# Kernel optimization log

Hardware: AMD Instinct MI355X
Metric: run time of the kernel (lower is better)

## Reference

```python
import jax, jax.numpy as jnp
import numpy as np
import math

B, N, E = 256, 512, 2048          # graphs, nodes per graph, edges per graph
EMB = 64                           # emb_sz (must be 64 to match final per-graph matmul with 64-d fc2 output)
NUM_ITEMS, NUM_CATS = 400000, 1000
RATIO = 0.9
EPS = 1e-5


def _bn(x, g, b):
    # BatchNorm1d in training mode: biased batch statistics
    m = x.mean(axis=0)
    v = x.var(axis=0)
    return g * (x - m) * jax.lax.rsqrt(v + EPS) + b


def _graph_conv(x, src, dst, emask, Wr, Wn, b):
    # PyG GraphConv, aggr='add': out_i = lin_root(x_i) + lin_rel(sum_{j->i} x_j) + bias
    msg = jnp.where(emask[:, None], x[src], jnp.zeros((), x.dtype))  # [E_tot, C]
    agg = jnp.zeros_like(x).at[dst].add(msg)
    return agg @ Wn + x @ Wr + b


def _topk_pool(x, src, dst, emask, p, n):
    # TopKPooling: score = x.p/||p||, keep top ceil(ratio*n) per graph, gate with tanh(score)
    k = int(math.ceil(RATIO * n))
    score = x @ p / jnp.linalg.norm(p)                       # [B*n]
    _, idx = jax.lax.top_k(score.reshape(B, n), k)           # [B, k] local indices
    gidx = (idx + (jnp.arange(B) * n)[:, None]).reshape(-1)  # [B*k] global indices
    xk = x[gidx] * jnp.tanh(score[gidx])[:, None]
    # remap edges; edges touching a dropped node become masked-out
    mapping = jnp.full((B * n,), -1, jnp.int32).at[gidx].set(jnp.arange(B * k, dtype=jnp.int32))
    nsrc, ndst = mapping[src], mapping[dst]
    valid = (nsrc >= 0) & (ndst >= 0) & emask
    return xk, jnp.maximum(nsrc, 0), jnp.maximum(ndst, 0), valid, k


def _readout(x, k):
    # uniform graphs: global_max_pool / global_mean_pool via reshape
    xg = x.reshape(B, k, -1)
    return jnp.concatenate([xg.max(axis=1), xg.mean(axis=1)], axis=1)  # [B, 256]


def setup_inputs() -> dict:
    key = jax.random.key(0)
    ks = jax.random.split(key, 32)
    nrm = jax.random.normal
    s = 0.02
    item_id = jax.random.randint(ks[0], (B * N,), 0, NUM_ITEMS)
    cat_id = jax.random.randint(ks[1], (B * N,), 0, NUM_CATS)
    off = (jnp.arange(B, dtype=jnp.int32) * N)[:, None]
    src = (jax.random.randint(ks[2], (B, E), 0, N, dtype=jnp.int32) + off).reshape(-1)
    dst = (jax.random.randint(ks[3], (B, E), 0, N, dtype=jnp.int32) + off).reshape(-1)
    d = dict(
        item_id=item_id, cat_id=cat_id, src=src, dst=dst,
        emb_item=nrm(ks[4], (NUM_ITEMS, EMB)) * s,
        emb_cat=nrm(ks[5], (NUM_CATS, EMB)) * s,
        W1r=nrm(ks[6], (2 * EMB, 128)) * s, W1n=nrm(ks[7], (2 * EMB, 128)) * s, b1=jnp.zeros(128), p1=nrm(ks[8], (128,)),
        W2r=nrm(ks[9], (128, 128)) * s, W2n=nrm(ks[10], (128, 128)) * s, b2=jnp.zeros(128), p2=nrm(ks[11], (128,)),
        W3r=nrm(ks[12], (128, 128)) * s, W3n=nrm(ks[13], (128, 128)) * s, b3=jnp.zeros(128), p3=nrm(ks[14], (128,)),
        fc1_W=nrm(ks[15], (256, 128)) * s, fc1_b=jnp.zeros(128), bn1_g=jnp.ones(128), bn1_b=jnp.zeros(128),
        fc2_W=nrm(ks[16], (128, 64)) * s, fc2_b=jnp.zeros(64), bn2_g=jnp.ones(64), bn2_b=jnp.zeros(64),
    )
    return d


def reference(item_id, cat_id, src, dst, emb_item, emb_cat,
              W1r, W1n, b1, p1, W2r, W2n, b2, p2, W3r, W3n, b3, p3,
              fc1_W, fc1_b, bn1_g, bn1_b, fc2_W, fc2_b, bn2_g, bn2_b):
    e_item = emb_item[item_id]                               # [B*N, 64]
    e_cat = emb_cat[cat_id]                                  # [B*N, 64]
    x = jnp.concatenate([e_item, e_cat], axis=1)             # [B*N, 128]
    emask = jnp.ones(src.shape, bool)

    x = jax.nn.relu(_graph_conv(x, src, dst, emask, W1r, W1n, b1))
    x, src, dst, emask, k1 = _topk_pool(x, src, dst, emask, p1, N)
    x1 = _readout(x, k1)

    x = jax.nn.relu(_graph_conv(x, src, dst, emask, W2r, W2n, b2))
    x, src, dst, emask, k2 = _topk_pool(x, src, dst, emask, p2, k1)
    x2 = _readout(x, k2)

    x = jax.nn.relu(_graph_conv(x, src, dst, emask, W3r, W3n, b3))
    x, src, dst, emask, k3 = _topk_pool(x, src, dst, emask, p3, k2)
    x3 = _readout(x, k3)

    g = x1 + x2 + x3                                         # [B, 256]
    g = jax.nn.relu(_bn(g @ fc1_W + fc1_b, bn1_g, bn1_b))    # fc1
    g = jax.nn.relu(_bn(g @ fc2_W + fc2_b, bn2_g, bn2_b))    # fc2
    # dropout is identity in eval; original applies relu again after dropout
    g = jax.nn.relu(g)                                       # [B, 64]
    # per-graph matmul loop: out[n] = <emb_item[n], g[graph_of_n]>; uniform graphs -> einsum
    out = jnp.einsum('bnd,bd->bn', e_item.reshape(B, N, EMB), g).reshape(-1)
    return jax.nn.sigmoid(out)                               # [B*N]
```

## Files before the change

### kernel.cpp

```cpp
#include <hip/hip_runtime.h>
#include <hip/hip_bf16.h>
#include <math.h>


#define TOTAL_NODES 131072
#define NUM_GRAPHS  256
#define NODES_PER_G 512
#define E_TOTAL     524288
#define EPG         2048
#define FDIM        128
#define EMBD        64

typedef __bf16 bf16x8 __attribute__((ext_vector_type(8)));
typedef float  f32x4  __attribute__((ext_vector_type(4)));

static __device__ __forceinline__ f32x4 mfma16(bf16x8 a, bf16x8 b, f32x4 c) {
  return __builtin_amdgcn_mfma_f32_16x16x32_bf16(a, b, c, 0, 0, 0);
}

static inline size_t align256(size_t x) { return (x + 255) & ~size_t(255); }

__global__ __launch_bounds__(256) void gather_embed_k(
    const int* __restrict__ item_id, const int* __restrict__ cat_id,
    const float* __restrict__ emb_item, const float* __restrict__ emb_cat,
    float* __restrict__ x, int total)
{
  int i = blockIdx.x * 256 + threadIdx.x;
  int node = i >> 5, part = i & 31;
  if (node >= total) return;
  float4 v;
  if (part < 16) {
    v = *(const float4*)&emb_item[(size_t)item_id[node] * EMBD + part * 4];
  } else {
    v = *(const float4*)&emb_cat[(size_t)cat_id[node] * EMBD + (part - 16) * 4];
  }
  *(float4*)&x[(size_t)node * FDIM + part * 4] = v;
}

__global__ __launch_bounds__(256) void wprep_k(
    const float* __restrict__ w0, const float* __restrict__ w1,
    const float* __restrict__ w2, const float* __restrict__ w3,
    const float* __restrict__ w4, const float* __restrict__ w5,
    __bf16* __restrict__ wout)
{
  const float* ws[6] = {w0, w1, w2, w3, w4, w5};
  int mat = blockIdx.y;
  int idx = blockIdx.x * 256 + threadIdx.x;
  int n = idx >> 7, k = idx & 127;
  float v = ws[mat][k * FDIM + n];
  __bf16 h = (__bf16)v;
  __bf16 l = (__bf16)(v - (float)h);
  __bf16* base = wout + (size_t)mat * 2 * 16384;
  base[idx] = h;
  base[16384 + idx] = l;
}

__global__ __launch_bounds__(128) void pnorm3_k(
    const float* __restrict__ p1, const float* __restrict__ p2,
    const float* __restrict__ p3, float* __restrict__ nrm)
{
  __shared__ float ss[128];
  const float* ps[3] = {p1, p2, p3};
  int t = threadIdx.x;
  for (int m = 0; m < 3; ++m) {
    float v = ps[m][t];
    ss[t] = v * v;
    __syncthreads();
    for (int s = 64; s > 0; s >>= 1) {
      if (t < s) ss[t] += ss[t + s];
      __syncthreads();
    }
    if (t == 0) nrm[m] = sqrtf(ss[0]);
    __syncthreads();
  }
}

__global__ __launch_bounds__(512) void csr_build1_k(
    const int* __restrict__ src_in, const int* __restrict__ dst_in,
    int* __restrict__ src_out, int* __restrict__ dst_out,
    int2* __restrict__ slot_pack, int* __restrict__ counts, int* __restrict__ offs)
{
  __shared__ int hist[512];
  __shared__ int scn[512];
  __shared__ int cur[512];
  const int b = blockIdx.x, t = threadIdx.x;
  const int ebase = b * EPG;
  const int nbase = b * NODES_PER_G;
  hist[t] = 0;
  __syncthreads();
  int so[4], ld[4];
#pragma unroll
  for (int i = 0; i < 4; ++i) {
    int e = ebase + t + i * 512;
    int s = src_in[e] - nbase;
    int d = dst_in[e] - nbase;
    src_out[e] = s; dst_out[e] = d;
    so[i] = s; ld[i] = d;
    atomicAdd(&hist[d], 1);
  }
  __syncthreads();
  int v = hist[t];
  scn[t] = v;
  __syncthreads();
  for (int dd = 1; dd < 512; dd <<= 1) {
    int add = (t >= dd) ? scn[t - dd] : 0;
    __syncthreads();
    scn[t] += add;
    __syncthreads();
  }
  {
    int excl = scn[t] - v;
    counts[nbase + t] = v;
    offs[nbase + t] = ebase + excl;
    cur[t] = excl;
  }
  __syncthreads();
#pragma unroll
  for (int i = 0; i < 4; ++i) {
    int pos = atomicAdd(&cur[ld[i]], 1);
    slot_pack[ebase + pos] = make_int2(nbase + so[i], __float_as_int(1.0f));
  }
}

__global__ __launch_bounds__(256) void gather_direct_k(
    const float* __restrict__ x, const int2* __restrict__ slot_pack,
    const int* __restrict__ off, const int* __restrict__ counts,
    float* __restrict__ agg, int M)
{
  int i = blockIdx.x * 256 + threadIdx.x;
  int node = i >> 5, lane = i & 31;
  if (node >= M) return;
  int deg = counts[node];
  int base = off[node];
  float4 a = make_float4(0.f, 0.f, 0.f, 0.f);
  for (int d = 0; d < deg; ++d) {
    int2 sp = slot_pack[base + d];
    float gt = __int_as_float(sp.y);
    float4 v = *(const float4*)&x[(size_t)sp.x * FDIM + lane * 4];
    a.x += gt * v.x; a.y += gt * v.y; a.z += gt * v.z; a.w += gt * v.w;
  }
  *(float4*)&agg[(size_t)node * FDIM + lane * 4] = a;
}

__global__ __launch_bounds__(256) void conv_mfma_k(
    const float* __restrict__ Asrc, const int* __restrict__ sel,
    const float* __restrict__ gates,
    const __bf16* __restrict__ W1hl,
    const float* __restrict__ A2,
    const __bf16* __restrict__ W2hl,
    const float* __restrict__ bias, const float* __restrict__ p,
    const float* __restrict__ nrm, float* __restrict__ C,
    float* __restrict__ score, int M)
{
  __shared__ __bf16 Wh[128 * 72];
  __shared__ __bf16 Wl[128 * 72];

  const int tid  = threadIdx.x;
  const int lane = tid & 63;
  const int w    = tid >> 6;
  const int row0 = blockIdx.x * 128;
  const int l15  = lane & 15;
  const int lg   = lane >> 4;

  f32x4 acc[2][8];
#pragma unroll
  for (int rf = 0; rf < 2; ++rf)
#pragma unroll
    for (int cf = 0; cf < 8; ++cf) acc[rf][cf] = (f32x4){0.f, 0.f, 0.f, 0.f};

  const int grow0 = row0 + w * 32 + l15;
  const int grow1 = grow0 + 16;

  for (int pass = 0; pass < 2; ++pass) {
    const float* __restrict__ A = pass ? A2 : Asrc;
    const __bf16* __restrict__ Whl = pass ? W2hl : W1hl;
    const bool use_sel = (pass == 0) && (sel != nullptr);
    int srow0 = use_sel ? sel[grow0] : grow0;
    int srow1 = use_sel ? sel[grow1] : grow1;
    float gt0 = use_sel ? gates[grow0] : 1.0f;
    float gt1 = use_sel ? gates[grow1] : 1.0f;

    for (int half = 0; half < 2; ++half) {
      const int k0 = half * 64;
      __syncthreads();
      for (int v = tid; v < 1024; v += 256) {
        int c = v >> 3, chn = (v & 7) * 8;
        *(bf16x8*)&Wh[c * 72 + chn] = *(const bf16x8*)&Whl[c * 128 + k0 + chn];
        *(bf16x8*)&Wl[c * 72 + chn] = *(const bf16x8*)&Whl[16384 + c * 128 + k0 + chn];
      }
      __syncthreads();

      bf16x8 ah[2][2], al[2][2];
#pragma unroll
      for (int rf = 0; rf < 2; ++rf) {
        int srow = rf ? srow1 : srow0;
        float gt = rf ? gt1 : gt0;
#pragma unroll
        for (int kc = 0; kc < 2; ++kc) {
          const float* ap = &A[(size_t)srow * FDIM + k0 + kc * 32 + lg * 8];
          float4 u0 = *(const float4*)ap;
          float4 u1 = *(const float4*)(ap + 4);
          float av[8] = {u0.x, u0.y, u0.z, u0.w, u1.x, u1.y, u1.z, u1.w};
#pragma unroll
          for (int j = 0; j < 8; ++j) {
            float vv = av[j] * gt;
            __bf16 h = (__bf16)vv;
            ah[rf][kc][j] = h;
            al[rf][kc][j] = (__bf16)(vv - (float)h);
          }
        }
      }
#pragma unroll
      for (int kc = 0; kc < 2; ++kc) {
        const int koff = kc * 32 + lg * 8;
#pragma unroll
        for (int cf = 0; cf < 8; ++cf) {
          const int bo = (cf * 16 + l15) * 72 + koff;
          bf16x8 bh = *(const bf16x8*)&Wh[bo];
          bf16x8 bl = *(const bf16x8*)&Wl[bo];
          acc[0][cf] = mfma16(ah[0][kc], bh, acc[0][cf]);
          acc[0][cf] = mfma16(ah[0][kc], bl, acc[0][cf]);
          acc[0][cf] = mfma16(al[0][kc], bh, acc[0][cf]);
          acc[1][cf] = mfma16(ah[1][kc], bh, acc[1][cf]);
          acc[1][cf] = mfma16(ah[1][kc], bl, acc[1][cf]);
          acc[1][cf] = mfma16(al[1][kc], bh, acc[1][cf]);
        }
      }
    }
  }

  const float nv = nrm[0];
  float bv[8], pv[8];
#pragma unroll
  for (int cf = 0; cf < 8; ++cf) {
    int col = cf * 16 + l15;
    bv[cf] = bias[col];
    pv[cf] = p[col];
  }
#pragma unroll
  for (int rf = 0; rf < 2; ++rf) {
#pragma unroll
    for (int j = 0; j < 4; ++j) {
      int row = row0 + w * 32 + rf * 16 + lg * 4 + j;
      float* crow = &C[(size_t)row * FDIM];
      float rsv = 0.f;
#pragma unroll
      for (int cf = 0; cf < 8; ++cf) {
        float val = acc[rf][cf][j] + bv[cf];
        val = fmaxf(val, 0.f);
        crow[cf * 16 + l15] = val;
        rsv += val * pv[cf];
      }
      rsv += __shfl_xor(rsv, 1, 16);
      rsv += __shfl_xor(rsv, 2, 16);
      rsv += __shfl_xor(rsv, 4, 16);
      rsv += __shfl_xor(rsv, 8, 16);
      if (l15 == 0) score[row] = rsv / nv;
    }
  }
}

__global__ __launch_bounds__(512) void pool_k(
    const float* __restrict__ score, const float* __restrict__ x,
    int n_old, int k_new,
    int* __restrict__ sel, float* __restrict__ gates,
    int* __restrict__ src_e, int* __restrict__ dst_e,
    int2* __restrict__ slot_pack, int* __restrict__ counts,
    int* __restrict__ offs, float* __restrict__ g)
{
  __shared__ float sv[512];
  __shared__ int   si[512];
  __shared__ int   map_[512];
  __shared__ float gl[512];
  __shared__ int   hist[512];
  __shared__ int   scn[512];
  __shared__ int   cur[512];
  __shared__ float rmx[4 * 128];
  __shared__ float rsm[4 * 128];
  const int b = blockIdx.x, t = threadIdx.x;
  const int nbase = b * n_old;
  sv[t] = (t < n_old) ? -score[nbase + t] : 3.0e38f;
  si[t] = t;
  __syncthreads();
  for (int kk = 2; kk <= 512; kk <<= 1) {
    for (int j = kk >> 1; j > 0; j >>= 1) {
      int ixj = t ^ j;
      if (ixj > t) {
        bool up = ((t & kk) == 0);
        float a = sv[t], c = sv[ixj];
        if ((a > c) == up) {
          sv[t] = c; sv[ixj] = a;
          int tmp = si[t]; si[t] = si[ixj]; si[ixj] = tmp;
        }
      }
      __syncthreads();
    }
  }
  if (t < n_old) {
    int o = si[t];
    if (t < k_new) {
      float gt = tanhf(-sv[t]);
      sel[b * k_new + t] = nbase + o;
      gates[b * k_new + t] = gt;
      gl[t] = gt;
      map_[o] = t;
    } else {
      map_[o] = -1;
    }
  }
  __syncthreads();
  if (slot_pack) {
    hist[t] = 0;
    __syncthreads();
    const int ebase = b * EPG;
    int so[4], ls[4], ld[4];
#pragma unroll
    for (int i = 0; i < 4; ++i) {
      int e = ebase + t + i * 512;
      int s = src_e[e], d = dst_e[e];
      so[i] = s;
      int ns = (s >= 0) ? map_[s] : -1;
      int nd = (d >= 0) ? map_[d] : -1;
      if (ns < 0 || nd < 0) { ns = -1; nd = -1; }
      src_e[e] = ns; dst_e[e] = nd;
      ls[i] = ns; ld[i] = nd;
      if (nd >= 0) atomicAdd(&hist[nd], 1);
    }
    __syncthreads();
    int v = (t < k_new) ? hist[t] : 0;
    scn[t] = v;
    __syncthreads();
    for (int dd = 1; dd < 512; dd <<= 1) {
      int add = (t >= dd) ? scn[t - dd] : 0;
      __syncthreads();
      scn[t] += add;
      __syncthreads();
    }
    if (t < k_new) {
      int excl = scn[t] - v;
      counts[b * k_new + t] = v;
      offs[b * k_new + t] = ebase + excl;
      cur[t] = excl;
    }
    __syncthreads();
#pragma unroll
    for (int i = 0; i < 4; ++i) {
      if (ld[i] >= 0) {
        int pos = atomicAdd(&cur[ld[i]], 1);
        slot_pack[ebase + pos] = make_int2(nbase + so[i], __float_as_int(gl[ls[i]]));
      }
    }
  }
  {
    const int col = t & 127;
    const int slot = t >> 7;
    float mx = -3.0e38f, sm = 0.f;
    for (int n = slot; n < k_new; n += 4) {
      int old = nbase + si[n];
      float v = x[(size_t)old * FDIM + col] * gl[n];
      mx = fmaxf(mx, v);
      sm += v;
    }
    rmx[slot * 128 + col] = mx;
    rsm[slot * 128 + col] = sm;
    __syncthreads();
    if (slot == 0) {
      float m0 = fmaxf(fmaxf(rmx[col], rmx[128 + col]),
                       fmaxf(rmx[256 + col], rmx[384 + col]));
      float s0 = rsm[col] + rsm[128 + col] + rsm[256 + col] + rsm[384 + col];
      g[b * 256 + col]       += m0;
      g[b * 256 + 128 + col] += s0 / (float)k_new;
    }
  }
}

__global__ __launch_bounds__(256) void head1_k(
    const float* __restrict__ g, const float* __restrict__ W,
    const float* __restrict__ bias, const float* __restrict__ gamma,
    const float* __restrict__ beta, float* __restrict__ h1)
{
  __shared__ float wsl[256 * 8];
  __shared__ float rsum[256 * 9];
  __shared__ float rsq[256 * 9];
  const int c0 = blockIdx.x * 8;
  const int t = threadIdx.x;
#pragma unroll
  for (int j = 0; j < 8; ++j) wsl[t * 8 + j] = W[t * 128 + c0 + j];
  __syncthreads();
  float acc[8] = {0.f, 0.f, 0.f, 0.f, 0.f, 0.f, 0.f, 0.f};
  const float* grow = &g[t * 256];
#pragma unroll
  for (int k = 0; k < 256; k += 4) {
    float4 gv = *(const float4*)&grow[k];
#pragma unroll
    for (int j = 0; j < 8; ++j) {
      acc[j] += gv.x * wsl[(k + 0) * 8 + j] + gv.y * wsl[(k + 1) * 8 + j]
              + gv.z * wsl[(k + 2) * 8 + j] + gv.w * wsl[(k + 3) * 8 + j];
    }
  }
#pragma unroll
  for (int j = 0; j < 8; ++j) {
    acc[j] += bias[c0 + j];
    rsum[t * 9 + j] = acc[j];
    rsq[t * 9 + j] = acc[j] * acc[j];
  }
  __syncthreads();
  for (int s = 128; s > 0; s >>= 1) {
    if (t < s) {
#pragma unroll
      for (int j = 0; j < 8; ++j) {
        rsum[t * 9 + j] += rsum[(t + s) * 9 + j];
        rsq[t * 9 + j]  += rsq[(t + s) * 9 + j];
      }
    }
    __syncthreads();
  }
#pragma unroll
  for (int j = 0; j < 8; ++j) {
    float m = rsum[j] * (1.f / 256.f);
    float var = rsq[j] * (1.f / 256.f) - m * m;
    float o = gamma[c0 + j] * (acc[j] - m) * rsqrtf(var + 1e-5f) + beta[c0 + j];
    h1[t * 128 + c0 + j] = fmaxf(o, 0.f);
  }
}

__global__ __launch_bounds__(256) void head2_k(
    const float* __restrict__ h1, const float* __restrict__ W,
    const float* __restrict__ bias, const float* __restrict__ gamma,
    const float* __restrict__ beta, float* __restrict__ h2)
{
  __shared__ float wsl[128 * 8];
  __shared__ float rsum[256 * 9];
  __shared__ float rsq[256 * 9];
  const int c0 = blockIdx.x * 8;
  const int t = threadIdx.x;
  if (t < 128) {
#pragma unroll
    for (int j = 0; j < 8; ++j) wsl[t * 8 + j] = W[t * 64 + c0 + j];
  }
  __syncthreads();
  float acc[8] = {0.f, 0.f, 0.f, 0.f, 0.f, 0.f, 0.f, 0.f};
  const float* hrow = &h1[t * 128];
#pragma unroll
  for (int k = 0; k < 128; k += 4) {
    float4 gv = *(const float4*)&hrow[k];
#pragma unroll
    for (int j = 0; j < 8; ++j) {
      acc[j] += gv.x * wsl[(k + 0) * 8 + j] + gv.y * wsl[(k + 1) * 8 + j]
              + gv.z * wsl[(k + 2) * 8 + j] + gv.w * wsl[(k + 3) * 8 + j];
    }
  }
#pragma unroll
  for (int j = 0; j < 8; ++j) {
    acc[j] += bias[c0 + j];
    rsum[t * 9 + j] = acc[j];
    rsq[t * 9 + j] = acc[j] * acc[j];
  }
  __syncthreads();
  for (int s = 128; s > 0; s >>= 1) {
    if (t < s) {
#pragma unroll
      for (int j = 0; j < 8; ++j) {
        rsum[t * 9 + j] += rsum[(t + s) * 9 + j];
        rsq[t * 9 + j]  += rsq[(t + s) * 9 + j];
      }
    }
    __syncthreads();
  }
#pragma unroll
  for (int j = 0; j < 8; ++j) {
    float m = rsum[j] * (1.f / 256.f);
    float var = rsq[j] * (1.f / 256.f) - m * m;
    float o = gamma[c0 + j] * (acc[j] - m) * rsqrtf(var + 1e-5f) + beta[c0 + j];
    h2[t * 64 + c0 + j] = fmaxf(o, 0.f);
  }
}

__global__ __launch_bounds__(256) void final_k(
    const float* __restrict__ x0, const float* __restrict__ g2,
    float* __restrict__ out, int total)
{
  int nid = blockIdx.x * 256 + threadIdx.x;
  if (nid >= total) return;
  int b = nid >> 9;
  const float* e = &x0[(size_t)nid * FDIM];
  const float* gg = &g2[(size_t)b * 64];
  float s = 0.f;
#pragma unroll
  for (int j = 0; j < 64; j += 4) {
    float4 a = *(const float4*)&e[j];
    float4 c = *(const float4*)&gg[j];
    s += a.x * c.x + a.y * c.y + a.z * c.z + a.w * c.w;
  }
  out[nid] = 1.f / (1.f + expf(-s));
}

extern "C" void kernel_launch(void* const* d_in, const int* in_sizes, int n_in,
                              void* d_out, int out_size, void* d_ws, size_t ws_size,
                              hipStream_t stream)
{
  const int*   item_id  = (const int*)  d_in[0];
  const int*   cat_id   = (const int*)  d_in[1];
  const int*   src_in   = (const int*)  d_in[2];
  const int*   dst_in   = (const int*)  d_in[3];
  const float* emb_item = (const float*)d_in[4];
  const float* emb_cat  = (const float*)d_in[5];
  const float* W1r = (const float*)d_in[6];
  const float* W1n = (const float*)d_in[7];
  const float* b1  = (const float*)d_in[8];
  const float* p1  = (const float*)d_in[9];
  const float* W2r = (const float*)d_in[10];
  const float* W2n = (const float*)d_in[11];
  const float* b2  = (const float*)d_in[12];
  const float* p2  = (const float*)d_in[13];
  const float* W3r = (const float*)d_in[14];
  const float* W3n = (const float*)d_in[15];
  const float* b3  = (const float*)d_in[16];
  const float* p3  = (const float*)d_in[17];
  const float* fc1_W = (const float*)d_in[18];
  const float* fc1_b = (const float*)d_in[19];
  const float* bn1_g = (const float*)d_in[20];
  const float* bn1_b = (const float*)d_in[21];
  const float* fc2_W = (const float*)d_in[22];
  const float* fc2_b = (const float*)d_in[23];
  const float* bn2_g = (const float*)d_in[24];
  const float* bn2_b = (const float*)d_in[25];
  float* out = (float*)d_out;

  const int TN = TOTAL_NODES;
  const int E  = E_TOTAL;
  const int k1 = 461, k2 = 415, k3 = 374;
  const int M1 = TN;
  const int M2 = NUM_GRAPHS * k1;
  const int M3 = NUM_GRAPHS * k2;

  char* ws = (char*)d_ws;
  size_t off = 0;
  auto carve = [&](size_t bytes) { char* p = ws + off; off += align256(bytes); return p; };
  float*  bufA   = (float*) carve((size_t)TN * FDIM * 4);
  float*  bufB   = (float*) carve((size_t)TN * FDIM * 4);
  float*  bufC   = (float*) carve((size_t)TN * FDIM * 4);
  float*  bufD   = (float*) carve((size_t)TN * FDIM * 4);
  float*  score  = (float*) carve((size_t)TN * 4);
  int*    sel    = (int*)   carve((size_t)TN * 4);
  float*  gates  = (float*) carve((size_t)TN * 4);
  int*    srcw   = (int*)   carve((size_t)E * 4);
  int*    dstw   = (int*)   carve((size_t)E * 4);
  int*    counts = (int*)   carve((size_t)TN * 4);
  int*    offs   = (int*)   carve((size_t)TN * 4);
  int2*   slotp  = (int2*)  carve((size_t)E * 8);
  __bf16* wbuf   = (__bf16*)carve(6 * 2 * 16384 * 2);
  float*  g      = (float*) carve(256 * 256 * 4);
  float*  h1     = (float*) carve(256 * 128 * 4);
  float*  h2     = (float*) carve(256 * 64 * 4);
  float*  nrm    = (float*) carve(256);
  if (off > ws_size) return;

  dim3 b256(256);
  auto blocks = [](long long work, int bs) { return dim3((unsigned)((work + bs - 1) / bs)); };

  const __bf16* W1r_hl = wbuf + 0 * 2 * 16384;
  const __bf16* W1n_hl = wbuf + 1 * 2 * 16384;
  const __bf16* W2r_hl = wbuf + 2 * 2 * 16384;
  const __bf16* W2n_hl = wbuf + 3 * 2 * 16384;
  const __bf16* W3r_hl = wbuf + 4 * 2 * 16384;
  const __bf16* W3n_hl = wbuf + 5 * 2 * 16384;

  hipMemsetAsync(g, 0, 256 * 256 * 4, stream);
  wprep_k<<<dim3(64, 6), b256, 0, stream>>>(W1r, W1n, W2r, W2n, W3r, W3n, wbuf);
  pnorm3_k<<<dim3(1), dim3(128), 0, stream>>>(p1, p2, p3, nrm);
  gather_embed_k<<<blocks((long long)TN * 32, 256), b256, 0, stream>>>(
      item_id, cat_id, emb_item, emb_cat, bufA, TN);

  csr_build1_k<<<dim3(NUM_GRAPHS), dim3(512), 0, stream>>>(
      src_in, dst_in, srcw, dstw, slotp, counts, offs);
  gather_direct_k<<<blocks((long long)M1 * 32, 256), b256, 0, stream>>>(
      bufA, slotp, offs, counts, bufB, M1);
  conv_mfma_k<<<dim3(M1 / 128), b256, 0, stream>>>(
      bufA, nullptr, nullptr, W1r_hl, bufB, W1n_hl, b1, p1, nrm + 0, bufC, score, M1);
  pool_k<<<dim3(NUM_GRAPHS), dim3(512), 0, stream>>>(
      score, bufC, NODES_PER_G, k1, sel, gates, srcw, dstw,
      slotp, counts, offs, g);

  gather_direct_k<<<blocks((long long)M2 * 32, 256), b256, 0, stream>>>(
      bufC, slotp, offs, counts, bufB, M2);
  conv_mfma_k<<<dim3(M2 / 128), b256, 0, stream>>>(
      bufC, sel, gates, W2r_hl, bufB, W2n_hl, b2, p2, nrm + 1, bufD, score, M2);
  pool_k<<<dim3(NUM_GRAPHS), dim3(512), 0, stream>>>(
      score, bufD, k1, k2, sel, gates, srcw, dstw,
      slotp, counts, offs, g);

  gather_direct_k<<<blocks((long long)M3 * 32, 256), b256, 0, stream>>>(
      bufD, slotp, offs, counts, bufB, M3);
  conv_mfma_k<<<dim3(M3 / 128), b256, 0, stream>>>(
      bufD, sel, gates, W3r_hl, bufB, W3n_hl, b3, p3, nrm + 2, bufC, score, M3);
  pool_k<<<dim3(NUM_GRAPHS), dim3(512), 0, stream>>>(
      score, bufC, k2, k3, sel, gates, nullptr, nullptr,
      nullptr, nullptr, nullptr, g);

  head1_k<<<dim3(16), b256, 0, stream>>>(g, fc1_W, fc1_b, bn1_g, bn1_b, h1);
  head2_k<<<dim3(8), b256, 0, stream>>>(h1, fc2_W, fc2_b, bn2_g, bn2_b, h2);

  final_k<<<blocks(TN, 256), b256, 0, stream>>>(bufA, h2, out, TN);
}
```

Baseline: 494.3 us.

## Split top-k pooling from readout and read conv weights directly from global memory

The fused pool kernel is split in two. A top-k/CSR kernel does only the sort and edge remap, and a new readout kernel uses a (graph, channel-chunk) grid with float4 loads and a shared-memory tree reduction for max and mean. The readout gathers rows through sel and gates instead of the sorted local indices. The conv MFMA kernel no longer stages the hi/lo bf16 weights in LDS and loads B fragments straight from global memory, relying on cache, which removes two barriers per half-pass. Conv outputs are written in place over the aggregation buffer, so one full-size workspace buffer is dropped. This adds an extra launch per layer and risks more global traffic for the weight fragments.

```diff
diff --git a/kernel.cpp b/kernel.cpp
--- a/kernel.cpp
+++ b/kernel.cpp
@@ -145,16 +145,13 @@
 __global__ __launch_bounds__(256) void conv_mfma_k(
     const float* __restrict__ Asrc, const int* __restrict__ sel,
     const float* __restrict__ gates,
-    const __bf16* __restrict__ W1hl,
+    const __bf16* __restrict__ Wr_hl,
     const float* __restrict__ A2,
-    const __bf16* __restrict__ W2hl,
+    const __bf16* __restrict__ Wn_hl,
     const float* __restrict__ bias, const float* __restrict__ p,
     const float* __restrict__ nrm, float* __restrict__ C,
     float* __restrict__ score, int M)
 {
-  __shared__ __bf16 Wh[128 * 72];
-  __shared__ __bf16 Wl[128 * 72];
-
   const int tid  = threadIdx.x;
   const int lane = tid & 63;
   const int w    = tid >> 6;
@@ -173,7 +170,7 @@
 
   for (int pass = 0; pass < 2; ++pass) {
     const float* __restrict__ A = pass ? A2 : Asrc;
-    const __bf16* __restrict__ Whl = pass ? W2hl : W1hl;
+    const __bf16* __restrict__ Whl = pass ? Wn_hl : Wr_hl;
     const bool use_sel = (pass == 0) && (sel != nullptr);
     int srow0 = use_sel ? sel[grow0] : grow0;
     int srow1 = use_sel ? sel[grow1] : grow1;
@@ -182,14 +179,6 @@
 
     for (int half = 0; half < 2; ++half) {
       const int k0 = half * 64;
-      __syncthreads();
-      for (int v = tid; v < 1024; v += 256) {
-        int c = v >> 3, chn = (v & 7) * 8;
-        *(bf16x8*)&Wh[c * 72 + chn] = *(const bf16x8*)&Whl[c * 128 + k0 + chn];
-        *(bf16x8*)&Wl[c * 72 + chn] = *(const bf16x8*)&Whl[16384 + c * 128 + k0 + chn];
-      }
-      __syncthreads();
-
       bf16x8 ah[2][2], al[2][2];
 #pragma unroll
       for (int rf = 0; rf < 2; ++rf) {
@@ -212,12 +201,12 @@
       }
 #pragma unroll
       for (int kc = 0; kc < 2; ++kc) {
-        const int koff = kc * 32 + lg * 8;
+        const int koff = k0 + kc * 32 + lg * 8;
 #pragma unroll
         for (int cf = 0; cf < 8; ++cf) {
-          const int bo = (cf * 16 + l15) * 72 + koff;
-          bf16x8 bh = *(const bf16x8*)&Wh[bo];
-          bf16x8 bl = *(const bf16x8*)&Wl[bo];
+          const __bf16* bp = &Whl[(size_t)(cf * 16 + l15) * 128 + koff];
+          bf16x8 bh = *(const bf16x8*)bp;
+          bf16x8 bl = *(const bf16x8*)(bp + 16384);
           acc[0][cf] = mfma16(ah[0][kc], bh, acc[0][cf]);
           acc[0][cf] = mfma16(ah[0][kc], bl, acc[0][cf]);
           acc[0][cf] = mfma16(al[0][kc], bh, acc[0][cf]);
@@ -260,13 +249,12 @@
   }
 }
 
-__global__ __launch_bounds__(512) void pool_k(
-    const float* __restrict__ score, const float* __restrict__ x,
-    int n_old, int k_new,
+__global__ __launch_bounds__(512) void topk_csr_k(
+    const float* __restrict__ score, int n_old, int k_new,
     int* __restrict__ sel, float* __restrict__ gates,
     int* __restrict__ src_e, int* __restrict__ dst_e,
     int2* __restrict__ slot_pack, int* __restrict__ counts,
-    int* __restrict__ offs, float* __restrict__ g)
+    int* __restrict__ offs)
 {
   __shared__ float sv[512];
   __shared__ int   si[512];
@@ -275,8 +263,6 @@
   __shared__ int   hist[512];
   __shared__ int   scn[512];
   __shared__ int   cur[512];
-  __shared__ float rmx[4 * 128];
-  __shared__ float rsm[4 * 128];
   const int b = blockIdx.x, t = threadIdx.x;
   const int nbase = b * n_old;
   sv[t] = (t < n_old) ? -score[nbase + t] : 3.0e38f;
@@ -309,7 +295,7 @@
     }
   }
   __syncthreads();
-  if (slot_pack) {
+  if (src_e) {
     hist[t] = 0;
     __syncthreads();
     const int ebase = b * EPG;
@@ -351,25 +337,55 @@
       }
     }
   }
-  {
-    const int col = t & 127;
-    const int slot = t >> 7;
-    float mx = -3.0e38f, sm = 0.f;
-    for (int n = slot; n < k_new; n += 4) {
-      int old = nbase + si[n];
-      float v = x[(size_t)old * FDIM + col] * gl[n];
-      mx = fmaxf(mx, v);
-      sm += v;
-    }
-    rmx[slot * 128 + col] = mx;
-    rsm[slot * 128 + col] = sm;
-    __syncthreads();
-    if (slot == 0) {
-      float m0 = fmaxf(fmaxf(rmx[col], rmx[128 + col]),
-                       fmaxf(rmx[256 + col], rmx[384 + col]));
-      float s0 = rsm[col] + rsm[128 + col] + rsm[256 + col] + rsm[384 + col];
-      g[b * 256 + col]       += m0;
-      g[b * 256 + 128 + col] += s0 / (float)k_new;
+}
+
+__global__ __launch_bounds__(256) void readout_k(
+    const float* __restrict__ x, const int* __restrict__ sel,
+    const float* __restrict__ gates, float* __restrict__ g, int k)
+{
+  __shared__ float lmx[32 * 36];
+  __shared__ float lsm[32 * 36];
+  const int b = blockIdx.x, ch = blockIdx.y;
+  const int c0 = ch * 32;
+  const int tid = threadIdx.x;
+  const int lane = tid & 7;
+  const int slot = tid >> 3;
+  float4 mx = make_float4(-3.0e38f, -3.0e38f, -3.0e38f, -3.0e38f);
+  float4 sm = make_float4(0.f, 0.f, 0.f, 0.f);
+  for (int n = slot; n < k; n += 32) {
+    int node = b * k + n;
+    int old = sel[node];
+    float gate = gates[node];
+    float4 v = *(const float4*)&x[(size_t)old * FDIM + c0 + lane * 4];
+    v.x *= gate; v.y *= gate; v.z *= gate; v.w *= gate;
+    mx.x = fmaxf(mx.x, v.x); mx.y = fmaxf(mx.y, v.y);
+    mx.z = fmaxf(mx.z, v.z); mx.w = fmaxf(mx.w, v.w);
+    sm.x += v.x; sm.y += v.y; sm.z += v.z; sm.w += v.w;
+  }
+  float* pm = &lmx[slot * 36 + lane * 4];
+  float* ps = &lsm[slot * 36 + lane * 4];
+  pm[0] = mx.x; pm[1] = mx.y; pm[2] = mx.z; pm[3] = mx.w;
+  ps[0] = sm.x; ps[1] = sm.y; ps[2] = sm.z; ps[3] = sm.w;
+  __syncthreads();
+  for (int s = 16; s > 0; s >>= 1) {
+    if (slot < s) {
+#pragma unroll
+      for (int j = 0; j < 4; ++j) {
+        int a = slot * 36 + lane * 4 + j;
+        int bb = (slot + s) * 36 + lane * 4 + j;
+        lmx[a] = fmaxf(lmx[a], lmx[bb]);
+        lsm[a] += lsm[bb];
+      }
+    }
+    __syncthreads();
+  }
+  if (slot == 0) {
+    float inv_k = 1.f / (float)k;
+#pragma unroll
+    for (int j = 0; j < 4; ++j) {
+      int c = c0 + lane * 4 + j;
+      g[b * 256 + c]       += lmx[lane * 4 + j];
+      g[b * 256 + 128 + c] += lsm[lane * 4 + j] * inv_k;
     }
   }
 }
@@ -540,7 +556,6 @@
   float*  bufA   = (float*) carve((size_t)TN * FDIM * 4);
   float*  bufB   = (float*) carve((size_t)TN * FDIM * 4);
   float*  bufC   = (float*) carve((size_t)TN * FDIM * 4);
-  float*  bufD   = (float*) carve((size_t)TN * FDIM * 4);
   float*  score  = (float*) carve((size_t)TN * 4);
   int*    sel    = (int*)   carve((size_t)TN * 4);
   float*  gates  = (float*) carve((size_t)TN * 4);
@@ -577,26 +592,26 @@
   gather_direct_k<<<blocks((long long)M1 * 32, 256), b256, 0, stream>>>(
       bufA, slotp, offs, counts, bufB, M1);
   conv_mfma_k<<<dim3(M1 / 128), b256, 0, stream>>>(
-      bufA, nullptr, nullptr, W1r_hl, bufB, W1n_hl, b1, p1, nrm + 0, bufC, score, M1);
-  pool_k<<<dim3(NUM_GRAPHS), dim3(512), 0, stream>>>(
-      score, bufC, NODES_PER_G, k1, sel, gates, srcw, dstw,
-      slotp, counts, offs, g);
+      bufA, nullptr, nullptr, W1r_hl, bufB, W1n_hl, b1, p1, nrm + 0, bufB, score, M1);
+  topk_csr_k<<<dim3(NUM_GRAPHS), dim3(512), 0, stream>>>(
+      score, NODES_PER_G, k1, sel, gates, srcw, dstw, slotp, counts, offs);
+  readout_k<<<dim3(NUM_GRAPHS, 4), b256, 0, stream>>>(bufB, sel, gates, g, k1);
 
   gather_direct_k<<<blocks((long long)M2 * 32, 256), b256, 0, stream>>>(
-      bufC, slotp, offs, counts, bufB, M2);
+      bufB, slotp, offs, counts, bufC, M2);
   conv_mfma_k<<<dim3(M2 / 128), b256, 0, stream>>>(
-      bufC, sel, gates, W2r_hl, bufB, W2n_hl, b2, p2, nrm + 1, bufD, score, M2);
-  pool_k<<<dim3(NUM_GRAPHS), dim3(512), 0, stream>>>(
-      score, bufD, k1, k2, sel, gates, srcw, dstw,
-      slotp, counts, offs, g);
+      bufB, sel, gates, W2r_hl, bufC, W2n_hl, b2, p2, nrm + 1, bufC, score, M2);
+  topk_csr_k<<<dim3(NUM_GRAPHS), dim3(512), 0, stream>>>(
+      score, k1, k2, sel, gates, srcw, dstw, slotp, counts, offs);
+  readout_k<<<dim3(NUM_GRAPHS, 4), b256, 0, stream>>>(bufC, sel, gates, g, k2);
 
   gather_direct_k<<<blocks((long long)M3 * 32, 256), b256, 0, stream>>>(
-      bufD, slotp, offs, counts, bufB, M3);
+      bufC, slotp, offs, counts, bufB, M3);
   conv_mfma_k<<<dim3(M3 / 128), b256, 0, stream>>>(
-      bufD, sel, gates, W3r_hl, bufB, W3n_hl, b3, p3, nrm + 2, bufC, score, M3);
-  pool_k<<<dim3(NUM_GRAPHS), dim3(512), 0, stream>>>(
-      score, bufC, k2, k3, sel, gates, nullptr, nullptr,
-      nullptr, nullptr, nullptr, g);
+      bufC, sel, gates, W3r_hl, bufB, W3n_hl, b3, p3, nrm + 2, bufB, score, M3);
+  topk_csr_k<<<dim3(NUM_GRAPHS), dim3(512), 0, stream>>>(
+      score, k2, k3, sel, gates, nullptr, nullptr, nullptr, nullptr, nullptr);
+  readout_k<<<dim3(NUM_GRAPHS, 4), b256, 0, stream>>>(bufB, sel, gates, g, k3);
 
   head1_k<<<dim3(16), b256, 0, stream>>>(g, fc1_W, fc1_b, bn1_g, bn1_b, h1);
   head2_k<<<dim3(8), b256, 0, stream>>>(h1, fc2_W, fc2_b, bn2_g, bn2_b, h2);
```

Result: slower. 519.4 us (+5.1%).
